# Kernel tuning notes

Measured on AMD Instinct MI355X. Metric: run time of the kernel, lower is better.

Reference implementation:

```python
import jax, jax.numpy as jnp
import numpy as np

EPS = 1e-20
K = 3  # kernel_size and max_pool_size


def _patches3(x):
    # x: [B,C,Hp,Wp] already padded by 1; returns [B,C,9,Hp-2,Wp-2] in torch-unfold kernel order
    H, W = x.shape[2] - 2, x.shape[3] - 2
    return jnp.stack([x[:, :, i:i + H, j:j + W] for i in range(3) for j in range(3)], axis=2)


def _pad1(x):
    return jnp.pad(x, ((0, 0), (0, 0), (1, 1), (1, 1)))


def _conv(x, w):
    return jax.lax.conv_general_dilated(x, w, (1, 1), ((1, 1), (1, 1)),
                                        dimension_numbers=('NCHW', 'OIHW', 'NCHW'))


def _prepare_weights(w_channel_d, w_spatial_d, w_pow_s, w_prop_s, w_channel_s, w_spatial_s):
    sp = jax.nn.softplus
    wcd, wsd, wcs, wss = sp(w_channel_d), sp(w_spatial_d), sp(w_channel_s), sp(w_spatial_s)
    wps = jax.nn.sigmoid(w_prop_s)
    wpow = sp(w_pow_s)
    # symmetric: mirror the first k//2 columns (k=3 -> 1 column)
    wsd = jnp.concatenate([wsd, wsd[:, :, :K // 2][:, :, ::-1]], axis=2)  # [i,3,3]
    wss = jnp.concatenate([wss, wss[:, :, :K // 2][:, :, ::-1]], axis=2)
    wcd = wcd / jnp.sum(wcd, axis=1, keepdims=True)
    wsd = wsd / jnp.sum(wsd, axis=(1, 2), keepdims=True)
    wcs = wcs / jnp.sum(wcs, axis=1, keepdims=True)
    wss = wss / jnp.sum(wss, axis=(1, 2), keepdims=True)
    w_conv_d = jnp.einsum('oi,ihw->oihw', wcd, wsd).reshape(wcd.shape[0], wcd.shape[1], K * K)  # [o,i,9]
    w_conv_s = jnp.einsum('oi,ihw->oihw', wcs, wss)  # [o,i,3,3]
    return w_conv_d, wps, wpow, w_conv_s


def setup_inputs() -> dict:
    key = jax.random.key(0)
    ks = jax.random.split(key, 9)
    B, C, H, W = 4, 1, 768, 768
    return {
        'x': jax.random.uniform(ks[0], (2 * B, C, H, W), dtype=jnp.float32),
        'scs': jax.random.uniform(ks[1], (B, C, H, W), dtype=jnp.float32),
        'cs': jax.random.uniform(ks[2], (B, C, H, W), dtype=jnp.float32),
        'w_channel_d': jnp.ones((1, 1), jnp.float32),
        'w_spatial_d': jax.random.uniform(ks[3], (1, 3, 2), dtype=jnp.float32),
        'w_pow_s': jax.random.uniform(ks[4], (1,), dtype=jnp.float32),
        'w_prop_s': jax.random.uniform(ks[5], (1,), dtype=jnp.float32),
        'w_channel_s': jnp.ones((1, 1), jnp.float32),
        'w_spatial_s': jax.random.uniform(ks[6], (1, 3, 2), dtype=jnp.float32),
    }


def reference(x, scs, cs, w_channel_d, w_spatial_d, w_pow_s, w_prop_s, w_channel_s, w_spatial_s):
    w_conv_d, wps, wpow, w_conv_s = _prepare_weights(
        w_channel_d, w_spatial_d, w_pow_s, w_prop_s, w_channel_s, w_spatial_s)
    B = cs.shape[0]
    dcd, cd = x[:B], x[B:]

    # stop-gradient pooling branch (torch uses .detach())
    dcd_sg, cd_sg = jax.lax.stop_gradient(dcd), jax.lax.stop_gradient(cd)
    d_pad = _pad1(dcd_sg / (cd_sg + EPS))
    cd_pad = _pad1(cd_sg)

    dp = _patches3(d_pad)   # [B,C,9,H,W]
    cp = _patches3(cd_pad)  # [B,C,9,H,W]
    j_max = jnp.argmax(dp * cp, axis=2)            # argmax of d*cd in each 3x3 window
    j_min = jnp.argmax(cp / (dp + EPS), axis=2)    # argmax of cd/d

    def _gather(p, j):
        return jnp.take_along_axis(p, j[:, :, None], axis=2)[:, :, 0]

    d_jmax, d_jmin = _gather(dp, j_max), _gather(dp, j_min)
    cd_jmax, cd_jmin = _gather(cp, j_max), _gather(cp, j_min)

    wpow_b = wpow.reshape(1, -1, 1, 1)  # n_in == 1
    wps_b = wps.reshape(1, -1, 1, 1)
    s_new = ((d_jmin + EPS) / (d_jmax + EPS)) ** wpow_b
    cs_new = cd_jmax * cd_jmin

    cs_out = _conv(cs * wps_b + cs_new * (1.0 - wps_b), w_conv_s)
    scs_out = _conv(scs * wps_b + s_new * cs_new * (1.0 - wps_b), w_conv_s)
    s = scs_out / (cs_out + EPS)

    # data-dependent per-pixel weights w_s: [B,C,9,H,W], center fixed to 1
    w_s = _patches3(_pad1(s)) * s[:, :, None]
    w_s = w_s.at[:, :, 4].set(1.0)

    ud = _patches3(_pad1(dcd))  # [B,C,9,H,W]
    uc = _patches3(_pad1(cd))
    num_d = jnp.einsum('bikhw,oik->bohw', ud * w_s, w_conv_d)
    num_c = jnp.einsum('bikhw,oik->bohw', uc * w_s, w_conv_d)
    den = jnp.einsum('bikhw,oik->bohw', w_s, w_conv_d) + EPS
    x_out = (jnp.stack((num_d, num_c), axis=1) / den[:, None]).reshape(2 * B, *s.shape[1:])
    return x_out, scs_out, cs_out
```

## Files before the change

### kernel.cpp

```cpp
#include <hip/hip_runtime.h>
#include <hip/hip_fp16.h>

#define EPSF 1e-20f

constexpr int Hh = 768, Ww = 768, Bb = 4;
constexpr int PLANE = Hh * Ww;
constexpr int TSX = 32, TSY = 24;
constexpr int R3Y = TSY + 6, R3X = TSX + 6;
constexpr int R2Y = TSY + 4, R2X = TSX + 4;
constexpr int R1Y = TSY + 2, R1X = TSX + 2;

__global__ __launch_bounds__(256)
void fused_all(const float* __restrict__ x, const float* __restrict__ scs,
               const float* __restrict__ cs,
               const float* __restrict__ w_sp_d, const float* __restrict__ w_sp_s,
               const float* __restrict__ w_pow_s, const float* __restrict__ w_prop_s,
               float* __restrict__ out) {
    __shared__ float2 s_qc[R3Y][R3X];
    __shared__ float2 s_t[R2Y][R2X];
    __shared__ __half s_s[R1Y][R1X];
    __shared__ float  sw[20];
    __shared__ float  swraw[18];

    const int orig = blockIdx.x;
    const int swz  = (orig & 7) * 384 + (orig >> 3);
    const int b    = swz / 768;
    const int rem  = swz - b * 768;
    const int ty0  = (rem / 24) * TSY;
    const int tx0  = (rem % 24) * TSX;

    const int tid = threadIdx.x;
    const float* dcd = x + b * PLANE;
    const float* cd  = x + (Bb + b) * PLANE;

    if (tid < 9) {
        int r = tid / 3, c = tid - r * 3;
        int cc = (c == 2) ? 0 : c;
        swraw[tid]     = log1pf(expf(w_sp_d[r * 2 + cc]));
        swraw[9 + tid] = log1pf(expf(w_sp_s[r * 2 + cc]));
    }
    if (tid == 9)  sw[18] = 1.f / (1.f + expf(-w_prop_s[0]));
    if (tid == 10) sw[19] = log1pf(expf(w_pow_s[0]));
    if (tid < 9) {
        float sum_d = 0.f, sum_s = 0.f;
        #pragma unroll
        for (int k = 0; k < 9; ++k) { sum_d += swraw[k]; sum_s += swraw[9 + k]; }
        sw[tid]     = swraw[tid]     / sum_d;
        sw[9 + tid] = swraw[9 + tid] / sum_s;
    }

    for (int it = tid; it < R3Y * 10; it += 256) {
        int row = it / 10, seg = it - row * 10;
        int gy = ty0 - 3 + row;
        int gxb = tx0 - 4 + seg * 4;
        float4 vd4 = make_float4(0.f, 0.f, 0.f, 0.f);
        float4 vc4 = vd4;
        if ((unsigned)gy < (unsigned)Hh) {
            bool safe = (seg > 0 && seg < 9) || (seg == 0 ? (tx0 > 0) : (tx0 + TSX < Ww));
            if (safe) {
                vd4 = *(const float4*)(dcd + gy * Ww + gxb);
                vc4 = *(const float4*)(cd  + gy * Ww + gxb);
            } else {
                if ((unsigned)(gxb + 0) < (unsigned)Ww) { vd4.x = dcd[gy*Ww+gxb+0]; vc4.x = cd[gy*Ww+gxb+0]; }
                if ((unsigned)(gxb + 1) < (unsigned)Ww) { vd4.y = dcd[gy*Ww+gxb+1]; vc4.y = cd[gy*Ww+gxb+1]; }
                if ((unsigned)(gxb + 2) < (unsigned)Ww) { vd4.z = dcd[gy*Ww+gxb+2]; vc4.z = cd[gy*Ww+gxb+2]; }
                if ((unsigned)(gxb + 3) < (unsigned)Ww) { vd4.w = dcd[gy*Ww+gxb+3]; vc4.w = cd[gy*Ww+gxb+3]; }
            }
        }
        int lxb = seg * 4 - 1;
        if ((unsigned)(lxb + 0) < (unsigned)R3X) s_qc[row][lxb + 0] = make_float2(vd4.x / (vc4.x + EPSF), vc4.x);
        if ((unsigned)(lxb + 1) < (unsigned)R3X) s_qc[row][lxb + 1] = make_float2(vd4.y / (vc4.y + EPSF), vc4.y);
        if ((unsigned)(lxb + 2) < (unsigned)R3X) s_qc[row][lxb + 2] = make_float2(vd4.z / (vc4.z + EPSF), vc4.z);
        if ((unsigned)(lxb + 3) < (unsigned)R3X) s_qc[row][lxb + 3] = make_float2(vd4.w / (vc4.w + EPSF), vc4.w);
    }

    const int xB = tid % R2X;
    const int tyB = tid / R2X;
    const int yb0 = tyB * 4;
    float pcs[4], pscs[4];
    if (tyB < 7) {
        int gx = tx0 - 2 + xB;
        bool colok = (unsigned)gx < (unsigned)Ww;
        #pragma unroll
        for (int j = 0; j < 4; ++j) {
            int gy = ty0 - 2 + yb0 + j;
            bool ok = colok && (unsigned)gy < (unsigned)Hh;
            int idx = ok ? (b * PLANE + gy * Ww + gx) : 0;
            pcs[j]  = ok ? cs[idx]  : 0.f;
            pscs[j] = ok ? scs[idx] : 0.f;
        }
    }
    __syncthreads();

    const float wps  = sw[18];
    const float wpow = sw[19];
    const float onemw = 1.f - wps;

    if (tyB < 7) {
        float ma[3], md[3], mc[3];
        float nv[3], nq[3];
#define HROW_B(rr, slot) { \
        float2 q0 = s_qc[rr][xB]; float2 q1 = s_qc[rr][xB + 1]; float2 q2 = s_qc[rr][xB + 2]; \
        float a0 = q0.x * q0.y, a1 = q1.x * q1.y, a2 = q2.x * q2.y; \
        float A = a0, D = q0.x, C = q0.y; \
        if (a1 > A) { A = a1; D = q1.x; C = q1.y; } \
        if (a2 > A) { A = a2; D = q2.x; C = q2.y; } \
        ma[slot] = A; md[slot] = D; mc[slot] = C; \
        float V = q0.y, Q = q0.x + EPSF; \
        float e1 = q1.x + EPSF, e2 = q2.x + EPSF; \
        if (q1.y * Q > V * e1) { V = q1.y; Q = e1; } \
        if (q2.y * Q > V * e2) { V = q2.y; Q = e2; } \
        nv[slot] = V; nq[slot] = Q; }
        HROW_B(yb0 + 0, 0)
        HROW_B(yb0 + 1, 1)
        #pragma unroll
        for (int j = 0; j < 4; ++j) {
            const int sl2 = (j + 2) % 3, s0 = j % 3, s1 = (j + 1) % 3;
            HROW_B(yb0 + j + 2, sl2)
            float A = ma[s0], D = md[s0], C = mc[s0];
            if (ma[s1]  > A) { A = ma[s1];  D = md[s1];  C = mc[s1];  }
            if (ma[sl2] > A) { A = ma[sl2]; D = md[sl2]; C = mc[sl2]; }
            float V = nv[s0], Q = nq[s0];
            if (nv[s1]  * Q > V * nq[s1])  { V = nv[s1];  Q = nq[s1];  }
            if (nv[sl2] * Q > V * nq[sl2]) { V = nv[sl2]; Q = nq[sl2]; }
            const int yb = yb0 + j;
            const int gy = ty0 - 2 + yb, gx = tx0 - 2 + xB;
            float tc = 0.f, ts = 0.f;
            if ((unsigned)gy < (unsigned)Hh && (unsigned)gx < (unsigned)Ww) {
                float s_new = __builtin_amdgcn_exp2f(wpow *
                    (__builtin_amdgcn_logf(Q) - __builtin_amdgcn_logf(D + EPSF)));
                float cs_new = C * V;
                tc = pcs[j]  * wps + cs_new * onemw;
                ts = pscs[j] * wps + s_new * cs_new * onemw;
            }
            s_t[yb][xB] = make_float2(tc, ts);
        }
    }
    __syncthreads();

    const int xC = tid % R1X;
    const int tyC = tid / R1X;
    const int yc0 = tyC * 4;
    float2 cres[4];
    if (tyC < 7) {
        const float wa0 = sw[9],  wb0 = sw[10];
        const float wa1 = sw[12], wb1 = sw[13];
        const float wa2 = sw[15], wb2 = sw[16];
        float2 u[3], tm[3];
#define HROW_C(rr, slot) { \
        float2 t0 = s_t[rr][xC]; float2 t1 = s_t[rr][xC + 1]; float2 t2 = s_t[rr][xC + 2]; \
        u[slot] = make_float2(t0.x + t2.x, t0.y + t2.y); tm[slot] = t1; }
        HROW_C(yc0 + 0, 0)
        HROW_C(yc0 + 1, 1)
        #pragma unroll
        for (int j = 0; j < 4; ++j) {
            const int yc = yc0 + j;
            if (yc < R1Y) {
                const int sl2 = (j + 2) % 3, s0 = j % 3, s1 = (j + 1) % 3;
                HROW_C(yc + 2, sl2)
                float accC = wa0 * u[s0].x + wb0 * tm[s0].x
                           + wa1 * u[s1].x + wb1 * tm[s1].x
                           + wa2 * u[sl2].x + wb2 * tm[sl2].x;
                float accS = wa0 * u[s0].y + wb0 * tm[s0].y
                           + wa1 * u[s1].y + wb1 * tm[s1].y
                           + wa2 * u[sl2].y + wb2 * tm[sl2].y;
                const int gy = ty0 - 1 + yc, gx = tx0 - 1 + xC;
                bool in_img = (unsigned)gy < (unsigned)Hh && (unsigned)gx < (unsigned)Ww;
                s_s[yc][xC] = __float2half(
                    in_img ? (accS * __builtin_amdgcn_rcpf(accC + EPSF)) : 0.f);
                cres[j] = make_float2(accC, accS);
            }
        }
    }
    __syncthreads();

    if (tyC < 7) {
        #pragma unroll
        for (int j = 0; j < 4; ++j) {
            const int yc = yc0 + j;
            if (yc < R1Y) s_t[yc][xC] = cres[j];
        }
    }
    __syncthreads();

    {
        const int xD = tid & 31, tyD = tid >> 5;
        const int yd0 = tyD * 3;
        float wdk[9];
        #pragma unroll
        for (int k = 0; k < 9; ++k) wdk[k] = sw[k];
        float  srw[3][3];
        float2 qrw[3][3];
#define HROW_D(rr, slot) { \
        srw[slot][0] = __half2float(s_s[rr][xD]); \
        srw[slot][1] = __half2float(s_s[rr][xD + 1]); \
        srw[slot][2] = __half2float(s_s[rr][xD + 2]); \
        qrw[slot][0] = s_qc[rr + 2][xD + 2]; qrw[slot][1] = s_qc[rr + 2][xD + 3]; qrw[slot][2] = s_qc[rr + 2][xD + 4]; }
        HROW_D(yd0 + 0, 0)
        HROW_D(yd0 + 1, 1)
#define TAP_D(slot, kk, cc2) { \
        float wsk = ((kk) == 4) ? 1.f : (srw[slot][cc2] * sc); \
        float w = wdk[kk] * wsk; \
        float2 q = qrw[slot][cc2]; \
        acc_d += w * (q.x * (q.y + EPSF)); \
        acc_c += w * q.y; \
        acc_w += w; }
        #pragma unroll
        for (int j = 0; j < 3; ++j) {
            const int sl2 = (j + 2) % 3, s0 = j % 3, s1 = (j + 1) % 3;
            HROW_D(yd0 + j + 2, sl2)
            float sc = srw[s1][1];
            float acc_d = 0.f, acc_c = 0.f, acc_w = 0.f;
            TAP_D(s0, 0, 0) TAP_D(s0, 1, 1) TAP_D(s0, 2, 2)
            TAP_D(s1, 3, 0) TAP_D(s1, 4, 1) TAP_D(s1, 5, 2)
            TAP_D(sl2, 6, 0) TAP_D(sl2, 7, 1) TAP_D(sl2, 8, 2)
            float rinv = __builtin_amdgcn_rcpf(acc_w + EPSF);
            const int iy = yd0 + j;
            int idx = (ty0 + iy) * Ww + (tx0 + xD);
            float2 cv = s_t[iy + 1][xD + 1];
            out[(2 * b)     * PLANE + idx] = acc_d * rinv;
            out[(2 * b + 1) * PLANE + idx] = acc_c * rinv;
            out[(8 + b)     * PLANE + idx] = cv.y;
            out[(12 + b)    * PLANE + idx] = cv.x;
        }
    }
}

extern "C" void kernel_launch(void* const* d_in, const int* in_sizes, int n_in,
                              void* d_out, int out_size, void* d_ws, size_t ws_size,
                              hipStream_t stream) {
    const float* x        = (const float*)d_in[0];
    const float* scs      = (const float*)d_in[1];
    const float* cs       = (const float*)d_in[2];
    const float* w_sp_d   = (const float*)d_in[4];
    const float* w_pow_s  = (const float*)d_in[5];
    const float* w_prop_s = (const float*)d_in[6];
    const float* w_sp_s   = (const float*)d_in[8];
    float* out  = (float*)d_out;

    fused_all<<<dim3(24 * 32 * Bb), 256, 0, stream>>>(x, scs, cs, w_sp_d, w_sp_s,
                                                      w_pow_s, w_prop_s, out);
}
```

Measured before the change: 30.50 us.

## Halve tile height to 12 rows with 128-thread blocks and factor center tap

Shrinks each tile from 32x24 to 32x12 and the block from 256 to 128 threads, doubling the grid and remapping the swizzle and per-thread row ranges (6 rows in stage B, 5 in stage C). This aims for more resident blocks and less per-block synchronisation stall, at the cost of a larger halo overhead ratio (18 vs 12 rows loaded per 12 output rows). The final weighted-average stage also factors the per-pixel center scale out of the eight non-center taps, using fmaf, to cut multiplies.

```diff
diff --git a/kernel.cpp b/kernel.cpp
--- a/kernel.cpp
+++ b/kernel.cpp
@@ -5,12 +5,12 @@
 
 constexpr int Hh = 768, Ww = 768, Bb = 4;
 constexpr int PLANE = Hh * Ww;
-constexpr int TSX = 32, TSY = 24;
+constexpr int TSX = 32, TSY = 12;
 constexpr int R3Y = TSY + 6, R3X = TSX + 6;
 constexpr int R2Y = TSY + 4, R2X = TSX + 4;
 constexpr int R1Y = TSY + 2, R1X = TSX + 2;
 
-__global__ __launch_bounds__(256)
+__global__ __launch_bounds__(128)
 void fused_all(const float* __restrict__ x, const float* __restrict__ scs,
                const float* __restrict__ cs,
                const float* __restrict__ w_sp_d, const float* __restrict__ w_sp_s,
@@ -23,9 +23,9 @@
     __shared__ float  swraw[18];
 
     const int orig = blockIdx.x;
-    const int swz  = (orig & 7) * 384 + (orig >> 3);
-    const int b    = swz / 768;
-    const int rem  = swz - b * 768;
+    const int swz  = (orig & 7) * 768 + (orig >> 3);
+    const int b    = swz / 1536;
+    const int rem  = swz - b * 1536;
     const int ty0  = (rem / 24) * TSY;
     const int tx0  = (rem % 24) * TSX;
 
@@ -49,7 +49,7 @@
         sw[9 + tid] = swraw[9 + tid] / sum_s;
     }
 
-    for (int it = tid; it < R3Y * 10; it += 256) {
+    for (int it = tid; it < R3Y * 10; it += 128) {
         int row = it / 10, seg = it - row * 10;
         int gy = ty0 - 3 + row;
         int gxb = tx0 - 4 + seg * 4;
@@ -76,15 +76,16 @@
 
     const int xB = tid % R2X;
     const int tyB = tid / R2X;
-    const int yb0 = tyB * 4;
-    float pcs[4], pscs[4];
-    if (tyB < 7) {
+    const int yb0 = tyB * 6;
+    float pcs[6], pscs[6];
+    if (tyB < 3) {
         int gx = tx0 - 2 + xB;
         bool colok = (unsigned)gx < (unsigned)Ww;
         #pragma unroll
-        for (int j = 0; j < 4; ++j) {
-            int gy = ty0 - 2 + yb0 + j;
-            bool ok = colok && (unsigned)gy < (unsigned)Hh;
+        for (int j = 0; j < 6; ++j) {
+            int yb = yb0 + j;
+            int gy = ty0 - 2 + yb;
+            bool ok = (yb < R2Y) && colok && (unsigned)gy < (unsigned)Hh;
             int idx = ok ? (b * PLANE + gy * Ww + gx) : 0;
             pcs[j]  = ok ? cs[idx]  : 0.f;
             pscs[j] = ok ? scs[idx] : 0.f;
@@ -96,7 +97,7 @@
     const float wpow = sw[19];
     const float onemw = 1.f - wps;
 
-    if (tyB < 7) {
+    if (tyB < 3) {
         float ma[3], md[3], mc[3];
         float nv[3], nq[3];
 #define HROW_B(rr, slot) { \
@@ -114,35 +115,37 @@
         HROW_B(yb0 + 0, 0)
         HROW_B(yb0 + 1, 1)
         #pragma unroll
-        for (int j = 0; j < 4; ++j) {
-            const int sl2 = (j + 2) % 3, s0 = j % 3, s1 = (j + 1) % 3;
-            HROW_B(yb0 + j + 2, sl2)
-            float A = ma[s0], D = md[s0], C = mc[s0];
-            if (ma[s1]  > A) { A = ma[s1];  D = md[s1];  C = mc[s1];  }
-            if (ma[sl2] > A) { A = ma[sl2]; D = md[sl2]; C = mc[sl2]; }
-            float V = nv[s0], Q = nq[s0];
-            if (nv[s1]  * Q > V * nq[s1])  { V = nv[s1];  Q = nq[s1];  }
-            if (nv[sl2] * Q > V * nq[sl2]) { V = nv[sl2]; Q = nq[sl2]; }
+        for (int j = 0; j < 6; ++j) {
             const int yb = yb0 + j;
-            const int gy = ty0 - 2 + yb, gx = tx0 - 2 + xB;
-            float tc = 0.f, ts = 0.f;
-            if ((unsigned)gy < (unsigned)Hh && (unsigned)gx < (unsigned)Ww) {
-                float s_new = __builtin_amdgcn_exp2f(wpow *
-                    (__builtin_amdgcn_logf(Q) - __builtin_amdgcn_logf(D + EPSF)));
-                float cs_new = C * V;
-                tc = pcs[j]  * wps + cs_new * onemw;
-                ts = pscs[j] * wps + s_new * cs_new * onemw;
+            if (yb < R2Y) {
+                const int sl2 = (j + 2) % 3, s0 = j % 3, s1 = (j + 1) % 3;
+                HROW_B(yb + 2, sl2)
+                float A = ma[s0], D = md[s0], C = mc[s0];
+                if (ma[s1]  > A) { A = ma[s1];  D = md[s1];  C = mc[s1];  }
+                if (ma[sl2] > A) { A = ma[sl2]; D = md[sl2]; C = mc[sl2]; }
+                float V = nv[s0], Q = nq[s0];
+                if (nv[s1]  * Q > V * nq[s1])  { V = nv[s1];  Q = nq[s1];  }
+                if (nv[sl2] * Q > V * nq[sl2]) { V = nv[sl2]; Q = nq[sl2]; }
+                const int gy = ty0 - 2 + yb, gx = tx0 - 2 + xB;
+                float tc = 0.f, ts = 0.f;
+                if ((unsigned)gy < (unsigned)Hh && (unsigned)gx < (unsigned)Ww) {
+                    float s_new = __builtin_amdgcn_exp2f(wpow *
+                        (__builtin_amdgcn_logf(Q) - __builtin_amdgcn_logf(D + EPSF)));
+                    float cs_new = C * V;
+                    tc = pcs[j]  * wps + cs_new * onemw;
+                    ts = pscs[j] * wps + s_new * cs_new * onemw;
+                }
+                s_t[yb][xB] = make_float2(tc, ts);
             }
-            s_t[yb][xB] = make_float2(tc, ts);
         }
     }
     __syncthreads();
 
     const int xC = tid % R1X;
     const int tyC = tid / R1X;
-    const int yc0 = tyC * 4;
-    float2 cres[4];
-    if (tyC < 7) {
+    const int yc0 = tyC * 5;
+    float2 cres[5];
+    if (tyC < 3) {
         const float wa0 = sw[9],  wb0 = sw[10];
         const float wa1 = sw[12], wb1 = sw[13];
         const float wa2 = sw[15], wb2 = sw[16];
@@ -153,7 +156,7 @@
         HROW_C(yc0 + 0, 0)
         HROW_C(yc0 + 1, 1)
         #pragma unroll
-        for (int j = 0; j < 4; ++j) {
+        for (int j = 0; j < 5; ++j) {
             const int yc = yc0 + j;
             if (yc < R1Y) {
                 const int sl2 = (j + 2) % 3, s0 = j % 3, s1 = (j + 1) % 3;
@@ -174,9 +177,9 @@
     }
     __syncthreads();
 
-    if (tyC < 7) {
-        #pragma unroll
-        for (int j = 0; j < 4; ++j) {
+    if (tyC < 3) {
+        #pragma unroll
+        for (int j = 0; j < 5; ++j) {
             const int yc = yc0 + j;
             if (yc < R1Y) s_t[yc][xC] = cres[j];
         }
@@ -198,28 +201,33 @@
         qrw[slot][0] = s_qc[rr + 2][xD + 2]; qrw[slot][1] = s_qc[rr + 2][xD + 3]; qrw[slot][2] = s_qc[rr + 2][xD + 4]; }
         HROW_D(yd0 + 0, 0)
         HROW_D(yd0 + 1, 1)
-#define TAP_D(slot, kk, cc2) { \
-        float wsk = ((kk) == 4) ? 1.f : (srw[slot][cc2] * sc); \
-        float w = wdk[kk] * wsk; \
+#define TAP_F(slot, kk, cc2) { \
+        float t = wdk[kk] * srw[slot][cc2]; \
         float2 q = qrw[slot][cc2]; \
-        acc_d += w * (q.x * (q.y + EPSF)); \
-        acc_c += w * q.y; \
-        acc_w += w; }
+        dn_p += t; \
+        nd_p = fmaf(t, q.x * (q.y + EPSF), nd_p); \
+        nc_p = fmaf(t, q.y, nc_p); }
         #pragma unroll
         for (int j = 0; j < 3; ++j) {
             const int sl2 = (j + 2) % 3, s0 = j % 3, s1 = (j + 1) % 3;
             HROW_D(yd0 + j + 2, sl2)
             float sc = srw[s1][1];
-            float acc_d = 0.f, acc_c = 0.f, acc_w = 0.f;
-            TAP_D(s0, 0, 0) TAP_D(s0, 1, 1) TAP_D(s0, 2, 2)
-            TAP_D(s1, 3, 0) TAP_D(s1, 4, 1) TAP_D(s1, 5, 2)
-            TAP_D(sl2, 6, 0) TAP_D(sl2, 7, 1) TAP_D(sl2, 8, 2)
-            float rinv = __builtin_amdgcn_rcpf(acc_w + EPSF);
+            float nd_p = 0.f, nc_p = 0.f, dn_p = 0.f;
+            TAP_F(s0, 0, 0) TAP_F(s0, 1, 1) TAP_F(s0, 2, 2)
+            TAP_F(s1, 3, 0)                 TAP_F(s1, 5, 2)
+            TAP_F(sl2, 6, 0) TAP_F(sl2, 7, 1) TAP_F(sl2, 8, 2)
+            const float w4 = wdk[4];
+            float2 q4 = qrw[s1][1];
+            float d4 = q4.x * (q4.y + EPSF);
+            float den = fmaf(sc, dn_p, w4) + EPSF;
+            float nd  = fmaf(sc, nd_p, w4 * d4);
+            float nc  = fmaf(sc, nc_p, w4 * q4.y);
+            float rinv = __builtin_amdgcn_rcpf(den);
             const int iy = yd0 + j;
             int idx = (ty0 + iy) * Ww + (tx0 + xD);
             float2 cv = s_t[iy + 1][xD + 1];
-            out[(2 * b)     * PLANE + idx] = acc_d * rinv;
-            out[(2 * b + 1) * PLANE + idx] = acc_c * rinv;
+            out[(2 * b)     * PLANE + idx] = nd * rinv;
+            out[(2 * b + 1) * PLANE + idx] = nc * rinv;
             out[(8 + b)     * PLANE + idx] = cv.y;
             out[(12 + b)    * PLANE + idx] = cv.x;
         }
@@ -238,6 +246,6 @@
     const float* w_sp_s   = (const float*)d_in[8];
     float* out  = (float*)d_out;
 
-    fused_all<<<dim3(24 * 32 * Bb), 256, 0, stream>>>(x, scs, cs, w_sp_d, w_sp_s,
+    fused_all<<<dim3(24 * 64 * Bb), 128, 0, stream>>>(x, scs, cs, w_sp_d, w_sp_s,
                                                       w_pow_s, w_prop_s, out);
 }
```

New measurement: 33.64 us. 10.3% more time.

## Split interior and edge tiles into templated kernels; factor center-pixel weight out of taps

Applied to the files above, without the earlier changes.

Templates the fused kernel on an EDGE flag and launches two grids: interior tiles with no bounds checks and unconditional float4 loads, and border tiles with the original checks. It also rewrites the final 9-tap weighted sum to factor the center scale out of the eight off-center taps using fmaf, saving multiplies. The cost is a second kernel launch and a smaller edge grid that may leave the GPU underused. The factored sum also changes floating-point rounding slightly.

```diff
diff --git a/kernel.cpp b/kernel.cpp
--- a/kernel.cpp
+++ b/kernel.cpp
@@ -10,12 +10,13 @@
 constexpr int R2Y = TSY + 4, R2X = TSX + 4;
 constexpr int R1Y = TSY + 2, R1X = TSX + 2;
 
+template<bool EDGE>
 __global__ __launch_bounds__(256)
-void fused_all(const float* __restrict__ x, const float* __restrict__ scs,
-               const float* __restrict__ cs,
-               const float* __restrict__ w_sp_d, const float* __restrict__ w_sp_s,
-               const float* __restrict__ w_pow_s, const float* __restrict__ w_prop_s,
-               float* __restrict__ out) {
+void fused_tile(const float* __restrict__ x, const float* __restrict__ scs,
+                const float* __restrict__ cs,
+                const float* __restrict__ w_sp_d, const float* __restrict__ w_sp_s,
+                const float* __restrict__ w_pow_s, const float* __restrict__ w_prop_s,
+                float* __restrict__ out) {
     __shared__ float2 s_qc[R3Y][R3X];
     __shared__ float2 s_t[R2Y][R2X];
     __shared__ __half s_s[R1Y][R1X];
@@ -23,11 +24,24 @@
     __shared__ float  swraw[18];
 
     const int orig = blockIdx.x;
-    const int swz  = (orig & 7) * 384 + (orig >> 3);
-    const int b    = swz / 768;
-    const int rem  = swz - b * 768;
-    const int ty0  = (rem / 24) * TSY;
-    const int tx0  = (rem % 24) * TSX;
+    int b, ty0, tx0;
+    if constexpr (!EDGE) {
+        const int swz = (orig & 7) * 330 + (orig >> 3);
+        b = swz / 660;
+        const int rem = swz - b * 660;
+        ty0 = (1 + rem / 22) * TSY;
+        tx0 = (1 + rem % 22) * TSX;
+    } else {
+        const int swz = (orig & 7) * 54 + (orig >> 3);
+        b = swz / 108;
+        const int rem = swz - b * 108;
+        int tyT, txT;
+        if (rem < 24)      { tyT = 0;  txT = rem; }
+        else if (rem < 48) { tyT = 31; txT = rem - 24; }
+        else if (rem < 78) { txT = 0;  tyT = 1 + (rem - 48); }
+        else               { txT = 23; tyT = 1 + (rem - 78); }
+        ty0 = tyT * TSY; tx0 = txT * TSX;
+    }
 
     const int tid = threadIdx.x;
     const float* dcd = x + b * PLANE;
@@ -53,18 +67,24 @@
         int row = it / 10, seg = it - row * 10;
         int gy = ty0 - 3 + row;
         int gxb = tx0 - 4 + seg * 4;
-        float4 vd4 = make_float4(0.f, 0.f, 0.f, 0.f);
-        float4 vc4 = vd4;
-        if ((unsigned)gy < (unsigned)Hh) {
-            bool safe = (seg > 0 && seg < 9) || (seg == 0 ? (tx0 > 0) : (tx0 + TSX < Ww));
-            if (safe) {
-                vd4 = *(const float4*)(dcd + gy * Ww + gxb);
-                vc4 = *(const float4*)(cd  + gy * Ww + gxb);
-            } else {
-                if ((unsigned)(gxb + 0) < (unsigned)Ww) { vd4.x = dcd[gy*Ww+gxb+0]; vc4.x = cd[gy*Ww+gxb+0]; }
-                if ((unsigned)(gxb + 1) < (unsigned)Ww) { vd4.y = dcd[gy*Ww+gxb+1]; vc4.y = cd[gy*Ww+gxb+1]; }
-                if ((unsigned)(gxb + 2) < (unsigned)Ww) { vd4.z = dcd[gy*Ww+gxb+2]; vc4.z = cd[gy*Ww+gxb+2]; }
-                if ((unsigned)(gxb + 3) < (unsigned)Ww) { vd4.w = dcd[gy*Ww+gxb+3]; vc4.w = cd[gy*Ww+gxb+3]; }
+        float4 vd4, vc4;
+        if constexpr (!EDGE) {
+            vd4 = *(const float4*)(dcd + gy * Ww + gxb);
+            vc4 = *(const float4*)(cd  + gy * Ww + gxb);
+        } else {
+            vd4 = make_float4(0.f, 0.f, 0.f, 0.f);
+            vc4 = vd4;
+            if ((unsigned)gy < (unsigned)Hh) {
+                bool safe = (seg > 0 && seg < 9) || (seg == 0 ? (tx0 > 0) : (tx0 + TSX < Ww));
+                if (safe) {
+                    vd4 = *(const float4*)(dcd + gy * Ww + gxb);
+                    vc4 = *(const float4*)(cd  + gy * Ww + gxb);
+                } else {
+                    if ((unsigned)(gxb + 0) < (unsigned)Ww) { vd4.x = dcd[gy*Ww+gxb+0]; vc4.x = cd[gy*Ww+gxb+0]; }
+                    if ((unsigned)(gxb + 1) < (unsigned)Ww) { vd4.y = dcd[gy*Ww+gxb+1]; vc4.y = cd[gy*Ww+gxb+1]; }
+                    if ((unsigned)(gxb + 2) < (unsigned)Ww) { vd4.z = dcd[gy*Ww+gxb+2]; vc4.z = cd[gy*Ww+gxb+2]; }
+                    if ((unsigned)(gxb + 3) < (unsigned)Ww) { vd4.w = dcd[gy*Ww+gxb+3]; vc4.w = cd[gy*Ww+gxb+3]; }
+                }
             }
         }
         int lxb = seg * 4 - 1;
@@ -80,14 +100,23 @@
     float pcs[4], pscs[4];
     if (tyB < 7) {
         int gx = tx0 - 2 + xB;
-        bool colok = (unsigned)gx < (unsigned)Ww;
-        #pragma unroll
-        for (int j = 0; j < 4; ++j) {
-            int gy = ty0 - 2 + yb0 + j;
-            bool ok = colok && (unsigned)gy < (unsigned)Hh;
-            int idx = ok ? (b * PLANE + gy * Ww + gx) : 0;
-            pcs[j]  = ok ? cs[idx]  : 0.f;
-            pscs[j] = ok ? scs[idx] : 0.f;
+        if constexpr (!EDGE) {
+            #pragma unroll
+            for (int j = 0; j < 4; ++j) {
+                int idx = b * PLANE + (ty0 - 2 + yb0 + j) * Ww + gx;
+                pcs[j]  = cs[idx];
+                pscs[j] = scs[idx];
+            }
+        } else {
+            bool colok = (unsigned)gx < (unsigned)Ww;
+            #pragma unroll
+            for (int j = 0; j < 4; ++j) {
+                int gy = ty0 - 2 + yb0 + j;
+                bool ok = colok && (unsigned)gy < (unsigned)Hh;
+                int idx = ok ? (b * PLANE + gy * Ww + gx) : 0;
+                pcs[j]  = ok ? cs[idx]  : 0.f;
+                pscs[j] = ok ? scs[idx] : 0.f;
+            }
         }
     }
     __syncthreads();
@@ -124,9 +153,14 @@
             if (nv[s1]  * Q > V * nq[s1])  { V = nv[s1];  Q = nq[s1];  }
             if (nv[sl2] * Q > V * nq[sl2]) { V = nv[sl2]; Q = nq[sl2]; }
             const int yb = yb0 + j;
-            const int gy = ty0 - 2 + yb, gx = tx0 - 2 + xB;
+            bool in_img;
+            if constexpr (!EDGE) in_img = true;
+            else {
+                const int gy = ty0 - 2 + yb, gx = tx0 - 2 + xB;
+                in_img = (unsigned)gy < (unsigned)Hh && (unsigned)gx < (unsigned)Ww;
+            }
             float tc = 0.f, ts = 0.f;
-            if ((unsigned)gy < (unsigned)Hh && (unsigned)gx < (unsigned)Ww) {
+            if (in_img) {
                 float s_new = __builtin_amdgcn_exp2f(wpow *
                     (__builtin_amdgcn_logf(Q) - __builtin_amdgcn_logf(D + EPSF)));
                 float cs_new = C * V;
@@ -164,8 +198,12 @@
                 float accS = wa0 * u[s0].y + wb0 * tm[s0].y
                            + wa1 * u[s1].y + wb1 * tm[s1].y
                            + wa2 * u[sl2].y + wb2 * tm[sl2].y;
-                const int gy = ty0 - 1 + yc, gx = tx0 - 1 + xC;
-                bool in_img = (unsigned)gy < (unsigned)Hh && (unsigned)gx < (unsigned)Ww;
+                bool in_img;
+                if constexpr (!EDGE) in_img = true;
+                else {
+                    const int gy = ty0 - 1 + yc, gx = tx0 - 1 + xC;
+                    in_img = (unsigned)gy < (unsigned)Hh && (unsigned)gx < (unsigned)Ww;
+                }
                 s_s[yc][xC] = __float2half(
                     in_img ? (accS * __builtin_amdgcn_rcpf(accC + EPSF)) : 0.f);
                 cres[j] = make_float2(accC, accS);
@@ -198,28 +236,33 @@
         qrw[slot][0] = s_qc[rr + 2][xD + 2]; qrw[slot][1] = s_qc[rr + 2][xD + 3]; qrw[slot][2] = s_qc[rr + 2][xD + 4]; }
         HROW_D(yd0 + 0, 0)
         HROW_D(yd0 + 1, 1)
-#define TAP_D(slot, kk, cc2) { \
-        float wsk = ((kk) == 4) ? 1.f : (srw[slot][cc2] * sc); \
-        float w = wdk[kk] * wsk; \
+#define TAP_F(slot, kk, cc2) { \
+        float t = wdk[kk] * srw[slot][cc2]; \
         float2 q = qrw[slot][cc2]; \
-        acc_d += w * (q.x * (q.y + EPSF)); \
-        acc_c += w * q.y; \
-        acc_w += w; }
+        dn_p += t; \
+        nd_p = fmaf(t, q.x * (q.y + EPSF), nd_p); \
+        nc_p = fmaf(t, q.y, nc_p); }
         #pragma unroll
         for (int j = 0; j < 3; ++j) {
             const int sl2 = (j + 2) % 3, s0 = j % 3, s1 = (j + 1) % 3;
             HROW_D(yd0 + j + 2, sl2)
             float sc = srw[s1][1];
-            float acc_d = 0.f, acc_c = 0.f, acc_w = 0.f;
-            TAP_D(s0, 0, 0) TAP_D(s0, 1, 1) TAP_D(s0, 2, 2)
-            TAP_D(s1, 3, 0) TAP_D(s1, 4, 1) TAP_D(s1, 5, 2)
-            TAP_D(sl2, 6, 0) TAP_D(sl2, 7, 1) TAP_D(sl2, 8, 2)
-            float rinv = __builtin_amdgcn_rcpf(acc_w + EPSF);
+            float nd_p = 0.f, nc_p = 0.f, dn_p = 0.f;
+            TAP_F(s0, 0, 0) TAP_F(s0, 1, 1) TAP_F(s0, 2, 2)
+            TAP_F(s1, 3, 0)                 TAP_F(s1, 5, 2)
+            TAP_F(sl2, 6, 0) TAP_F(sl2, 7, 1) TAP_F(sl2, 8, 2)
+            const float w4 = wdk[4];
+            float2 q4 = qrw[s1][1];
+            float d4 = q4.x * (q4.y + EPSF);
+            float den = fmaf(sc, dn_p, w4) + EPSF;
+            float nd  = fmaf(sc, nd_p, w4 * d4);
+            float nc  = fmaf(sc, nc_p, w4 * q4.y);
+            float rinv = __builtin_amdgcn_rcpf(den);
             const int iy = yd0 + j;
             int idx = (ty0 + iy) * Ww + (tx0 + xD);
             float2 cv = s_t[iy + 1][xD + 1];
-            out[(2 * b)     * PLANE + idx] = acc_d * rinv;
-            out[(2 * b + 1) * PLANE + idx] = acc_c * rinv;
+            out[(2 * b)     * PLANE + idx] = nd * rinv;
+            out[(2 * b + 1) * PLANE + idx] = nc * rinv;
             out[(8 + b)     * PLANE + idx] = cv.y;
             out[(12 + b)    * PLANE + idx] = cv.x;
         }
@@ -238,6 +281,8 @@
     const float* w_sp_s   = (const float*)d_in[8];
     float* out  = (float*)d_out;
 
-    fused_all<<<dim3(24 * 32 * Bb), 256, 0, stream>>>(x, scs, cs, w_sp_d, w_sp_s,
+    fused_tile<false><<<dim3(2640), 256, 0, stream>>>(x, scs, cs, w_sp_d, w_sp_s,
                                                       w_pow_s, w_prop_s, out);
+    fused_tile<true><<<dim3(432), 256, 0, stream>>>(x, scs, cs, w_sp_d, w_sp_s,
+                                                    w_pow_s, w_prop_s, out);
 }
```

Result: slower. 35.66 us (+16.9%).
